# Kernel tuning notes

Hardware: AMD Instinct MI355X
Metric: run time of the kernel (lower is better)

The kernel has to match this reference:

```python
import jax, jax.numpy as jnp
import numpy as np
from math import sqrt

D_MODEL = 1024
HEADS = 16
D_K = D_MODEL // HEADS
NEG = -1e9


def setup_inputs() -> dict:
    key = jax.random.key(0)
    ks = jax.random.split(key, 8)
    bs, s, d = 2, 2048, D_MODEL
    inp = {
        "k": jax.random.normal(ks[0], (bs, s, d), jnp.float32),
        "v": jax.random.normal(ks[1], (bs, s, d), jnp.float32),
        "q": jax.random.normal(ks[2], (bs, s, d), jnp.float32),
        "mask": jax.random.randint(ks[3], (bs, s, 1), 0, 2).astype(jnp.int64),
        # torch nn.Linear weights: y = x @ W.T, W is [out, in]
        "Wq": jax.random.normal(ks[4], (d, d), jnp.float32) / sqrt(d),
        "Wk": jax.random.normal(ks[5], (d, d), jnp.float32) / sqrt(d),
        "Wv": jax.random.normal(ks[6], (d, d), jnp.float32) / sqrt(d),
        "Wo": jax.random.normal(ks[7], (d, d), jnp.float32) / sqrt(d),
    }
    return inp


def reference(k, v, q, mask, Wq, Wk, Wv, Wo):
    bs, s_k, d = k.shape
    s_q = q.shape[1]
    h, d_k = HEADS, D_K
    # linear projections (no bias), then split heads -> [bs, h, s, d_k]
    kh = (k @ Wk.T).reshape(bs, s_k, h, d_k).transpose(0, 2, 1, 3)
    vh = (v @ Wv.T).reshape(bs, s_k, h, d_k).transpose(0, 2, 1, 3)
    qh = (q @ Wq.T).reshape(bs, s_q, h, d_k).transpose(0, 2, 1, 3)
    # scaled dot-product scores [bs, h, s_q, s_k]
    scores = jnp.einsum("bhqd,bhkd->bhqk", qh, kh) / sqrt(d_k)
    # mask [bs, s_k, 1] -> [bs, 1, 1, s_k], masked positions get -1e9
    m = mask[:, None].transpose(0, 1, 3, 2)  # [bs,1,1,s_k]
    scores = jnp.where(m == 0, NEG, scores)
    probs = jax.nn.softmax(scores, axis=-1)  # dropout is identity (eval)
    attn = jnp.einsum("bhqk,bhkd->bhqd", probs, vh)
    attn_concat = attn.transpose(0, 2, 1, 3).reshape(bs, s_q, d)
    return attn_concat @ Wo.T
```

## Files before the change

### kernel.cpp

```cpp
#include <hip/hip_runtime.h>

typedef __bf16 bf16x8 __attribute__((ext_vector_type(8)));
typedef float f32x4 __attribute__((ext_vector_type(4)));

#define BS 2
#define SEQ 2048
#define DM 1024
#define NH 16
#define DKH 64
#define GM 4096
#define GN 1024
#define GK 1024
#define NEGV (-1e9f)

#define OFF_XQ 0u
#define OFF_XK 4194304u
#define OFF_XV 8388608u
#define OFF_WQ 12582912u
#define OFF_WK 13631488u
#define OFF_WV 14680064u
#define OFF_WO 15728640u
#define OFF_QH 16777216u
#define OFF_KC 20971520u
#define OFF_VT 25165824u
#define OFF_AT OFF_XQ

#if __has_builtin(__builtin_amdgcn_exp2f)
#define EXP2(x) __builtin_amdgcn_exp2f(x)
#else
static __device__ __forceinline__ float EXP2(float x) {
    float r;
    asm volatile("v_exp_f32 %0, %1" : "=v"(r) : "v"(x));
    return r;
}
#endif

__device__ __forceinline__ unsigned cvt_pk(float lo, float hi) {
    unsigned r;
    asm volatile("v_cvt_pk_bf16_f32 %0, %1, %2" : "=v"(r) : "v"(lo), "v"(hi));
    return r;
}

__device__ __forceinline__ unsigned short f2b(float f) {
    unsigned u = __builtin_bit_cast(unsigned, f);
    u += 0x7fffu + ((u >> 16) & 1u);
    return (unsigned short)(u >> 16);
}

typedef const __attribute__((address_space(1))) unsigned int* gas_t;
typedef __attribute__((address_space(3))) unsigned int* las_t;

__device__ __forceinline__ void gload_lds16(const ushort* g, ushort* l) {
    __builtin_amdgcn_global_load_lds((gas_t)(const void*)g, (las_t)(void*)l, 16, 0, 0);
}

#define BARRIER() __builtin_amdgcn_s_barrier()
#define VMCNT(n) asm volatile("s_waitcnt vmcnt(" #n ")" ::: "memory")

__global__ __launch_bounds__(256)
void cvt_scan(const float* __restrict__ q, const float* __restrict__ k,
              const float* __restrict__ v, const float* __restrict__ wq,
              const float* __restrict__ wk, const float* __restrict__ wv,
              const float* __restrict__ wo, ushort* __restrict__ ws,
              const int* __restrict__ mask, int* __restrict__ cpos,
              int* __restrict__ mbuf)
{
    const int tid = threadIdx.x;
    if (blockIdx.y == 7) {
        if (blockIdx.x >= 2) return;
        const int b = blockIdx.x;
        const int* mp = mask + (size_t)b * SEQ;
        const int lane = tid & 63, w = tid >> 6;
        int vv[8];
        int cnt = 0;
#pragma unroll
        for (int j = 0; j < 8; ++j) { vv[j] = mp[tid * 8 + j]; cnt += (vv[j] != 0); }
        int inc = cnt;
#pragma unroll
        for (int d = 1; d < 64; d <<= 1) {
            int t = __shfl_up(inc, d);
            if (lane >= d) inc += t;
        }
        __shared__ int wsum[4];
        if (lane == 63) wsum[w] = inc;
        __syncthreads();
        int base = inc - cnt;
        for (int i = 0; i < w; ++i) base += wsum[i];
        int c = base;
        int* ob = cpos + (size_t)b * SEQ;
#pragma unroll
        for (int j = 0; j < 8; ++j) {
            ob[tid * 8 + j] = (vv[j] != 0) ? c : -1;
            c += (vv[j] != 0);
        }
        if (tid == 255) mbuf[b] = base + cnt;
        return;
    }
    const float* src; unsigned n; unsigned dst;
    switch (blockIdx.y) {
        case 0: src = q;  n = 4194304u; dst = OFF_XQ; break;
        case 1: src = k;  n = 4194304u; dst = OFF_XK; break;
        case 2: src = v;  n = 4194304u; dst = OFF_XV; break;
        case 3: src = wq; n = 1048576u; dst = OFF_WQ; break;
        case 4: src = wk; n = 1048576u; dst = OFF_WK; break;
        case 5: src = wv; n = 1048576u; dst = OFF_WV; break;
        default: src = wo; n = 1048576u; dst = OFF_WO; break;
    }
    unsigned i = (blockIdx.x * 256u + tid) * 8u;
    if (i >= n) return;
    float4 f0 = *(const float4*)(src + i);
    float4 f1 = *(const float4*)(src + i + 4);
    uint4 o;
    o.x = cvt_pk(f0.x, f0.y);
    o.y = cvt_pk(f0.z, f0.w);
    o.z = cvt_pk(f1.x, f1.y);
    o.w = cvt_pk(f1.z, f1.w);
    *(uint4*)(ws + dst + i) = o;
}

__global__ __launch_bounds__(256)
void gemm256(const ushort* __restrict__ Abase, const ushort* __restrict__ Bbase,
             ushort* __restrict__ wsbase, const int* __restrict__ cpos)
{
    __shared__ __align__(16) ushort pool[4][2][2][4096];

    const unsigned z = blockIdx.y;
    const ushort* A  = Abase + (size_t)z * (GM * GK);
    const ushort* Bw = Bbase + (size_t)z * (GN * GK);
    const float scale = (z == 0) ? 0.125f * 1.44269504088896f : 1.0f;

    const int tid = threadIdx.x;
    const int lane = tid & 63, wid = tid >> 6;
    const int lr = lane & 15, lg = lane >> 4;
    const int grow = lane >> 3, gseg = lane & 7;

    const int lin = blockIdx.x;
    const int xcd = lin & 7, kid = lin >> 3;
    const int mi = xcd * 2 + (kid >> 4), ni = kid & 15;
    const int m0 = mi * 256 + wid * 64;
    const int n0 = ni * 64;

    ushort* lA[2] = { &pool[wid][0][0][0], &pool[wid][1][0][0] };
    ushort* lB[2] = { &pool[wid][0][1][0], &pool[wid][1][1][0] };

    f32x4 acc[4][4] = {};

    auto STAGE = [&](int s, int t) {
        const int k0 = t * 64;
#pragma unroll
        for (int g = 0; g < 8; ++g) {
            int row = g * 8 + grow;
            gload_lds16(A + (size_t)(m0 + row) * GK + k0 + ((gseg ^ (row & 7)) * 8),
                        lA[s] + g * 512);
            gload_lds16(Bw + (size_t)(n0 + row) * GK + k0 + ((gseg ^ (row & 7)) * 8),
                        lB[s] + g * 512);
        }
    };

    STAGE(0, 0);
    STAGE(1, 1);

    for (int t = 0; t < 16; ++t) {
        const int s = t & 1;
        if (t < 15) { VMCNT(16); } else { VMCNT(0); }
        const ushort* la = lA[s];
        const ushort* lb = lB[s];
        bf16x8 af[2][4], bfr[2][4];
#pragma unroll
        for (int kk = 0; kk < 2; ++kk)
#pragma unroll
            for (int i = 0; i < 4; ++i) {
                int ra = i * 16 + lr;
                int off = ra * 64 + (((kk * 4 + lg) ^ (ra & 7)) * 8);
                af[kk][i]  = *(const bf16x8*)&la[off];
                bfr[kk][i] = *(const bf16x8*)&lb[off];
            }
        __builtin_amdgcn_s_setprio(1);
#pragma unroll
        for (int kk = 0; kk < 2; ++kk)
#pragma unroll
            for (int i = 0; i < 4; ++i)
#pragma unroll
                for (int j = 0; j < 4; ++j)
                    acc[i][j] = __builtin_amdgcn_mfma_f32_16x16x32_bf16(
                        af[kk][i], bfr[kk][j], acc[i][j], 0, 0, 0);
        __builtin_amdgcn_s_setprio(0);
        if (t + 2 < 16) STAGE(s, t + 2);
    }

    ushort* qh  = wsbase + OFF_QH;
    ushort* kc  = wsbase + OFF_KC;
    ushort* vtp = wsbase + OFF_VT;
#pragma unroll
    for (int i = 0; i < 4; ++i) {
#pragma unroll
        for (int r = 0; r < 4; ++r) {
            int row = m0 + i * 16 + lg * 4 + r;
            int b = row >> 11, s = row & 2047;
            if (z == 0) {
#pragma unroll
                for (int j = 0; j < 4; ++j) {
                    int col = n0 + j * 16 + lr;
                    qh[(((size_t)b * NH + (col >> 6)) * SEQ + s) * DKH + (col & 63)] =
                        f2b(acc[i][j][r] * scale);
                }
            } else {
                int c = cpos[b * SEQ + s];
                if (c >= 0) {
                    if (z == 1) {
#pragma unroll
                        for (int j = 0; j < 4; ++j) {
                            int col = n0 + j * 16 + lr;
                            kc[(((size_t)b * NH + (col >> 6)) * SEQ + c) * DKH + (col & 63)] =
                                f2b(acc[i][j][r]);
                        }
                    } else {
                        int vt = (c & ~63) | ((c & 15) * 4 + ((c >> 4) & 3));
#pragma unroll
                        for (int j = 0; j < 4; ++j) {
                            int col = n0 + j * 16 + lr;
                            vtp[(((size_t)b * NH + (col >> 6)) * DKH + (col & 63)) * SEQ + vt] =
                                f2b(acc[i][j][r]);
                        }
                    }
                }
            }
        }
    }
}

__global__ __launch_bounds__(256)
void gemm_bt(const ushort* __restrict__ A, const ushort* __restrict__ Bw,
             float* __restrict__ of)
{
    __shared__ __align__(16) ushort lA[2][128 * 64];
    __shared__ __align__(16) ushort lB[2][128 * 64];

    const int tid = threadIdx.x;
    const int lane = tid & 63, wid = tid >> 6;
    const int wr = wid >> 1, wc = wid & 1;
    const int lr = lane & 15, lg = lane >> 4;
    const int lin = blockIdx.y * 8 + blockIdx.x;
    const int swz = (lin & 7) * 32 + (lin >> 3);
    const int m0 = (swz >> 3) * 128, n0 = (swz & 7) * 128;
    const int srow8 = lane >> 3, scol = lane & 7;

    f32x4 acc[4][4] = {};
    bf16x8 af[2][4], bfr[2][4];

#define OSTAGE(s, t)                                                               \
    _Pragma("unroll") for (int p = 0; p < 4; ++p) {                                \
        int r = wid * 32 + p * 8 + srow8;                                          \
        gload_lds16(A + (size_t)(m0 + r) * GK + (t) * 64 + ((scol ^ (r & 7)) * 8), \
                    &lA[s][(wid * 32 + p * 8) * 64]);                              \
        gload_lds16(Bw + (size_t)(n0 + r) * GK + (t) * 64 + ((scol ^ (r & 7)) * 8),\
                    &lB[s][(wid * 32 + p * 8) * 64]);                              \
    }
#define OLDX(s)                                                                    \
    _Pragma("unroll") for (int kk = 0; kk < 2; ++kk)                               \
    _Pragma("unroll") for (int i = 0; i < 4; ++i) {                                \
        int ra = wr * 64 + i * 16 + lr;                                            \
        af[kk][i] = *(const bf16x8*)&lA[s][ra * 64 + (((kk * 4 + lg) ^ (ra & 7)) * 8)];  \
        int rb = wc * 64 + i * 16 + lr;                                            \
        bfr[kk][i] = *(const bf16x8*)&lB[s][rb * 64 + (((kk * 4 + lg) ^ (rb & 7)) * 8)]; \
    }
#define OMMA()                                                                     \
    __builtin_amdgcn_s_setprio(1);                                                 \
    _Pragma("unroll") for (int kk = 0; kk < 2; ++kk)                               \
    _Pragma("unroll") for (int i = 0; i < 4; ++i)                                  \
    _Pragma("unroll") for (int j = 0; j < 4; ++j)                                  \
        acc[i][j] = __builtin_amdgcn_mfma_f32_16x16x32_bf16(af[kk][i], bfr[kk][j], \
                                                            acc[i][j], 0, 0, 0);   \
    __builtin_amdgcn_s_setprio(0);

    OSTAGE(0, 0);
    __syncthreads();

    for (int t = 0; t < 16; ++t) {
        const int cur = t & 1;
        if (t + 1 < 16) OSTAGE(cur ^ 1, t + 1);
        OLDX(cur);
        OMMA();
        __syncthreads();
    }

#pragma unroll
    for (int i = 0; i < 4; ++i)
#pragma unroll
        for (int j = 0; j < 4; ++j) {
            int col = n0 + wc * 64 + j * 16 + lr;
#pragma unroll
            for (int r = 0; r < 4; ++r) {
                int row = m0 + wr * 64 + i * 16 + lg * 4 + r;
                of[(size_t)row * GN + col] = acc[i][j][r];
            }
        }
#undef OSTAGE
#undef OLDX
#undef OMMA
}

__global__ __launch_bounds__(256)
void attn_kernel(ushort* __restrict__ ws, const int* __restrict__ mbuf)
{
    const int bid = blockIdx.x;
    const int qt = bid & 15;
    const int h  = (bid >> 4) & 15;
    const int b  = bid >> 8;
    const int bh = b * NH + h;

    const ushort* Qp = ws + OFF_QH + (size_t)bh * (SEQ * DKH);
    const ushort* Kc = ws + OFF_KC + (size_t)bh * (SEQ * DKH);
    const ushort* VT = ws + OFF_VT + (size_t)bh * (DKH * SEQ);
    ushort* At = ws + OFF_AT;

    const int mb = mbuf[b];
    const int nt = (mb + 63) >> 6;

    __shared__ __align__(16) ushort lK[3][64 * 64];
    __shared__ __align__(16) ushort lV[3][64 * 64];
    __shared__ __align__(16) ushort lP[4][32][72];

    const int tid = threadIdx.x;
    const int lane = tid & 63, wid = tid >> 6;
    const int lr = lane & 15, lg = lane >> 4;
    ushort* lPw = &lP[wid][0][0];

    const int srow = wid * 16 + (lane >> 3);
    const int sg = lane & 7;

    const int qrow0 = qt * 128 + wid * 32;
    bf16x8 qf[2][2];
#pragma unroll
    for (int fr = 0; fr < 2; ++fr)
#pragma unroll
        for (int kk = 0; kk < 2; ++kk)
            qf[fr][kk] = *(const bf16x8*)(Qp + (size_t)(qrow0 + fr * 16 + lr) * DKH + kk * 32 + lg * 8);

    f32x4 acc_o[2][4] = {};
    float lrun[2][4] = {};

    auto STAGE = [&](int buf, int kt) {
        const int kbase = kt * 64;
#pragma unroll
        for (int c = 0; c < 2; ++c) {
            int r = srow + c * 8;
            gload_lds16(Kc + (size_t)(kbase + r) * DKH + ((sg ^ (r & 7)) * 8),
                        &lK[buf][(wid * 16 + c * 8) * 64]);
            gload_lds16(VT + (size_t)r * SEQ + kbase + ((sg ^ (r & 7)) * 8),
                        &lV[buf][(wid * 16 + c * 8) * 64]);
        }
    };

    STAGE(0, 0);
    if (nt > 1) STAGE(1, 1);

    int slot = 0;
    for (int kt = 0; kt < nt; ++kt) {
        if (kt + 1 < nt) { VMCNT(4); } else { VMCNT(0); }
        BARRIER();
        if (kt + 2 < nt) {
            int s2 = slot + 2; if (s2 >= 3) s2 -= 3;
            STAGE(s2, kt + 2);
        }
        const ushort* lKc = lK[slot];
        const ushort* lVc = lV[slot];

        f32x4 s[2][4];
        __builtin_amdgcn_s_setprio(1);
#pragma unroll
        for (int fc = 0; fc < 4; ++fc) {
            int row = fc * 16 + lr;
            int sw = row & 7;
            bf16x8 kf0 = *(const bf16x8*)(lKc + row * 64 + ((lg ^ sw) * 8));
            bf16x8 kf1 = *(const bf16x8*)(lKc + row * 64 + (((4 + lg) ^ sw) * 8));
#pragma unroll
            for (int fr = 0; fr < 2; ++fr) {
                f32x4 t = {};
                t = __builtin_amdgcn_mfma_f32_16x16x32_bf16(qf[fr][0], kf0, t, 0, 0, 0);
                t = __builtin_amdgcn_mfma_f32_16x16x32_bf16(qf[fr][1], kf1, t, 0, 0, 0);
                s[fr][fc] = t;
            }
        }
        __builtin_amdgcn_s_setprio(0);

        if (kt == nt - 1) {
            const int kbase = kt * 64;
#pragma unroll
            for (int fc = 0; fc < 4; ++fc)
                if (kbase + fc * 16 + lr >= mb)
#pragma unroll
                    for (int fr = 0; fr < 2; ++fr)
                        s[fr][fc] = f32x4{NEGV, NEGV, NEGV, NEGV};
        }

#pragma unroll
        for (int fr = 0; fr < 2; ++fr)
#pragma unroll
            for (int r = 0; r < 4; ++r) {
                float p0 = EXP2(s[fr][0][r]), p1 = EXP2(s[fr][1][r]);
                float p2 = EXP2(s[fr][2][r]), p3 = EXP2(s[fr][3][r]);
                lrun[fr][r] += (p0 + p1) + (p2 + p3);
                uint2 pk;
                pk.x = cvt_pk(p0, p1);
                pk.y = cvt_pk(p2, p3);
                *(uint2*)(lPw + (fr * 16 + lg * 4 + r) * 72 + lr * 4) = pk;
            }

        __builtin_amdgcn_s_setprio(1);
#pragma unroll
        for (int kk = 0; kk < 2; ++kk) {
            bf16x8 pf[2];
#pragma unroll
            for (int fr = 0; fr < 2; ++fr)
                pf[fr] = *(const bf16x8*)(lPw + (fr * 16 + lr) * 72 + kk * 32 + lg * 8);
#pragma unroll
            for (int fc2 = 0; fc2 < 4; ++fc2) {
                int d = fc2 * 16 + lr;
                bf16x8 vf = *(const bf16x8*)(lVc + d * 64 + (((kk * 4 + lg) ^ (d & 7)) * 8));
#pragma unroll
                for (int fr = 0; fr < 2; ++fr)
                    acc_o[fr][fc2] = __builtin_amdgcn_mfma_f32_16x16x32_bf16(pf[fr], vf, acc_o[fr][fc2], 0, 0, 0);
            }
        }
        __builtin_amdgcn_s_setprio(0);

        ++slot; if (slot >= 3) slot -= 3;
    }

#pragma unroll
    for (int fr = 0; fr < 2; ++fr)
#pragma unroll
        for (int r = 0; r < 4; ++r) {
            float l = lrun[fr][r];
            l += __shfl_xor(l, 1);
            l += __shfl_xor(l, 2);
            l += __shfl_xor(l, 4);
            l += __shfl_xor(l, 8);
            float rl = 1.0f / l;
            int qrow = qrow0 + fr * 16 + lg * 4 + r;
#pragma unroll
            for (int fc2 = 0; fc2 < 4; ++fc2)
                At[((size_t)(b * SEQ) + qrow) * DM + h * DKH + fc2 * 16 + lr] =
                    f2b(acc_o[fr][fc2][r] * rl);
        }
}

extern "C" void kernel_launch(void* const* d_in, const int* in_sizes, int n_in,
                              void* d_out, int out_size, void* d_ws, size_t ws_size,
                              hipStream_t stream) {
    const float* kin = (const float*)d_in[0];
    const float* vin = (const float*)d_in[1];
    const float* qin = (const float*)d_in[2];
    const int*   msk = (const int*)d_in[3];
    const float* wq  = (const float*)d_in[4];
    const float* wk  = (const float*)d_in[5];
    const float* wv  = (const float*)d_in[6];
    const float* wo  = (const float*)d_in[7];
    ushort* ws = (ushort*)d_ws;
    float* out = (float*)d_out;
    int* cposb = (int*)d_out;
    int* mbuf = cposb + BS * SEQ;

    cvt_scan<<<dim3(2048, 8), 256, 0, stream>>>(qin, kin, vin, wq, wk, wv, wo,
                                                ws, msk, cposb, mbuf);
    gemm256<<<dim3(256, 3), 256, 0, stream>>>(ws + OFF_XQ, ws + OFF_WQ, ws, cposb);
    attn_kernel<<<512, 256, 0, stream>>>(ws, mbuf);
    gemm_bt<<<dim3(8, 32), 256, 0, stream>>>(ws + OFF_AT, ws + OFF_WO, out);
}
```

Measured before the change: 116.8 us.

## Retile projection GEMM to share A rows per block and stream A into registers

The projection GEMM tile is remapped so all four waves of a block share the same 64 rows of A and cover different 64-column slices of B, forming a 64x256 block tile. A fragments are now loaded straight from global memory into registers with double buffering. Only B is staged through LDS, which halves the shared-memory footprint, and the K loop is unrolled in pairs to overlap the loads with MFMA work. The intent is to cut LDS traffic and pressure, at the cost of uncoalesced direct global reads of A that depend on cache reuse across the waves, plus extra register use.

After: 137.7 us. 1.18x slower.

```diff
diff --git a/kernel.cpp b/kernel.cpp
--- a/kernel.cpp
+++ b/kernel.cpp
@@ -122,7 +122,7 @@
 void gemm256(const ushort* __restrict__ Abase, const ushort* __restrict__ Bbase,
              ushort* __restrict__ wsbase, const int* __restrict__ cpos)
 {
-    __shared__ __align__(16) ushort pool[4][2][2][4096];
+    __shared__ __align__(16) ushort poolB[4][2][4096];
 
     const unsigned z = blockIdx.y;
     const ushort* A  = Abase + (size_t)z * (GM * GK);
@@ -136,45 +136,43 @@
 
     const int lin = blockIdx.x;
     const int xcd = lin & 7, kid = lin >> 3;
-    const int mi = xcd * 2 + (kid >> 4), ni = kid & 15;
-    const int m0 = mi * 256 + wid * 64;
-    const int n0 = ni * 64;
-
-    ushort* lA[2] = { &pool[wid][0][0][0], &pool[wid][1][0][0] };
-    ushort* lB[2] = { &pool[wid][0][1][0], &pool[wid][1][1][0] };
+    const int mi = xcd * 8 + (kid & 7), ni = kid >> 3;
+    const int m0 = mi * 64;
+    const int n0 = ni * 256 + wid * 64;
+
+    ushort* lB0 = &poolB[wid][0][0];
+    ushort* lB1 = &poolB[wid][1][0];
 
     f32x4 acc[4][4] = {};
-
-    auto STAGE = [&](int s, int t) {
+    bf16x8 a0[2][4], a1[2][4], bfr[2][4];
+
+    auto STAGEB = [&](ushort* dst, int t) {
         const int k0 = t * 64;
 #pragma unroll
         for (int g = 0; g < 8; ++g) {
             int row = g * 8 + grow;
-            gload_lds16(A + (size_t)(m0 + row) * GK + k0 + ((gseg ^ (row & 7)) * 8),
-                        lA[s] + g * 512);
             gload_lds16(Bw + (size_t)(n0 + row) * GK + k0 + ((gseg ^ (row & 7)) * 8),
-                        lB[s] + g * 512);
+                        dst + g * 512);
         }
     };
-
-    STAGE(0, 0);
-    STAGE(1, 1);
-
-    for (int t = 0; t < 16; ++t) {
-        const int s = t & 1;
-        if (t < 15) { VMCNT(16); } else { VMCNT(0); }
-        const ushort* la = lA[s];
-        const ushort* lb = lB[s];
-        bf16x8 af[2][4], bfr[2][4];
+    auto LOADA = [&](bf16x8 (&d)[2][4], int t) {
+        const int k0 = t * 64;
 #pragma unroll
         for (int kk = 0; kk < 2; ++kk)
 #pragma unroll
+            for (int i = 0; i < 4; ++i)
+                d[kk][i] = *(const bf16x8*)(A + (size_t)(m0 + i * 16 + lr) * GK + k0 + (kk * 4 + lg) * 8);
+    };
+    auto RDB = [&](const ushort* l) {
+#pragma unroll
+        for (int kk = 0; kk < 2; ++kk)
+#pragma unroll
             for (int i = 0; i < 4; ++i) {
-                int ra = i * 16 + lr;
-                int off = ra * 64 + (((kk * 4 + lg) ^ (ra & 7)) * 8);
-                af[kk][i]  = *(const bf16x8*)&la[off];
-                bfr[kk][i] = *(const bf16x8*)&lb[off];
-            }
+                int rb = i * 16 + lr;
+                bfr[kk][i] = *(const bf16x8*)&l[rb * 64 + (((kk * 4 + lg) ^ (rb & 7)) * 8)];
+            }
+    };
+    auto MMA = [&](bf16x8 (&a)[2][4]) {
         __builtin_amdgcn_s_setprio(1);
 #pragma unroll
         for (int kk = 0; kk < 2; ++kk)
@@ -183,9 +181,28 @@
 #pragma unroll
                 for (int j = 0; j < 4; ++j)
                     acc[i][j] = __builtin_amdgcn_mfma_f32_16x16x32_bf16(
-                        af[kk][i], bfr[kk][j], acc[i][j], 0, 0, 0);
+                        a[kk][i], bfr[kk][j], acc[i][j], 0, 0, 0);
         __builtin_amdgcn_s_setprio(0);
-        if (t + 2 < 16) STAGE(s, t + 2);
+    };
+
+    LOADA(a0, 0);
+    STAGEB(lB0, 0);
+    STAGEB(lB1, 1);
+    VMCNT(8);
+
+#pragma unroll
+    for (int tt = 0; tt < 8; ++tt) {
+        const int t0 = 2 * tt, t1 = 2 * tt + 1;
+        if (t0 > 0) { VMCNT(16); }
+        RDB(lB0);
+        MMA(a0);
+        LOADA(a1, t1);
+        if (t0 + 2 < 16) STAGEB(lB0, t0 + 2);
+        if (t1 == 15) { VMCNT(8); } else { VMCNT(16); }
+        RDB(lB1);
+        MMA(a1);
+        if (t1 + 1 < 16) LOADA(a0, t1 + 1);
+        if (t1 + 2 < 16) STAGEB(lB1, t1 + 2);
     }
 
     ushort* qh  = wsbase + OFF_QH;
```
